# Optimization experiments

Measured on AMD Instinct MI355X. Metric: run time of the kernel, lower is better.

Reference implementation:

```python
import jax, jax.numpy as jnp
import numpy as np

TREE_DEPTH = 10
TOTAL = 2 ** (TREE_DEPTH + 1) - 1  # 2047 nodes per tree
G = 64                              # graphs per batch
N = G * TOTAL                       # 131008 nodes
E = 2 * N                           # 262016 directed edges
H = 256                             # h_dim
HALF = H // 2
L = 4                               # num_layers
LABELS = 32
OUT = 32
BN_EPS = 1e-5
LN_EPS = 1e-5


def setup_inputs() -> dict:
    key = jax.random.key(0)
    ks = jax.random.split(key, 16)
    x = jnp.stack([jax.random.randint(ks[0], (N,), 0, TOTAL),
                   jax.random.randint(ks[1], (N,), 0, LABELS)], axis=1)
    edge_src = jax.random.randint(ks[2], (E,), 0, N)
    edge_dst = jax.random.randint(ks[3], (E,), 0, N)
    edge_weight = jax.random.uniform(ks[4], (E,), dtype=jnp.float32)
    batch = jnp.arange(N, dtype=jnp.int64) // TOTAL          # node -> graph id
    root_index = jnp.arange(G, dtype=jnp.int64) * TOTAL      # one root per graph
    s = 0.02
    emb_node = jax.random.normal(ks[5], (TOTAL, HALF), dtype=jnp.float32) * s
    emb_label = jax.random.normal(ks[6], (LABELS, HALF), dtype=jnp.float32) * s
    w = 1.0 / np.sqrt(H)
    W1 = jax.random.normal(ks[7], (L, H, H), dtype=jnp.float32) * w
    b1 = jnp.zeros((L, H), dtype=jnp.float32)
    g1 = jnp.ones((L, H), dtype=jnp.float32)
    be1 = jnp.zeros((L, H), dtype=jnp.float32)
    W2 = jax.random.normal(ks[8], (L, H, H), dtype=jnp.float32) * w
    b2 = jnp.zeros((L, H), dtype=jnp.float32)
    g2 = jnp.ones((L, H), dtype=jnp.float32)
    be2 = jnp.zeros((L, H), dtype=jnp.float32)
    ln_g = jnp.ones((L, H), dtype=jnp.float32)
    ln_b = jnp.zeros((L, H), dtype=jnp.float32)
    Wout = jax.random.normal(ks[9], (OUT, H), dtype=jnp.float32) * w
    return {"x": x, "edge_src": edge_src, "edge_dst": edge_dst,
            "edge_weight": edge_weight, "batch": batch, "root_index": root_index,
            "emb_node": emb_node, "emb_label": emb_label,
            "W1": W1, "b1": b1, "g1": g1, "be1": be1,
            "W2": W2, "b2": b2, "g2": g2, "be2": be2,
            "ln_g": ln_g, "ln_b": ln_b, "Wout": Wout}


def _batchnorm(h, g, b):
    # BatchNorm1d, training-mode batch statistics over the node dim
    m = h.mean(axis=0)
    v = h.var(axis=0)
    return g * (h - m) * jax.lax.rsqrt(v + BN_EPS) + b


def _layernorm(h, g, b):
    m = h.mean(axis=-1, keepdims=True)
    v = h.var(axis=-1, keepdims=True)
    return g * (h - m) * jax.lax.rsqrt(v + LN_EPS) + b


def reference(x, edge_src, edge_dst, edge_weight, batch, root_index,
              emb_node, emb_label, W1, b1, g1, be1, W2, b2, g2, be2,
              ln_g, ln_b, Wout):
    # BiEmbedding_cat: concat of two h/2 embeddings
    h = jnp.concatenate([emb_node[x[:, 0]], emb_label[x[:, 1]]], axis=-1)  # [N,H]
    target_roots = root_index[batch]  # all-nodes->root targets for last layer
    for i in range(L):
        if i == L - 1:  # last_layer_fully_adjacent: every node sends to its root
            agg = jnp.zeros_like(h).at[target_roots].add(h)
        else:
            agg = jnp.zeros_like(h).at[edge_dst].add(h[edge_src] * edge_weight[:, None])
        m = h + agg  # GIN with eps=0: (1+eps)*x + sum_j w_ij x_j
        m = jax.nn.relu(_batchnorm(m @ W1[i].T + b1[i], g1[i], be1[i]))
        m = jax.nn.relu(_batchnorm(m @ W2[i].T + b2[i], g2[i], be2[i]))
        # use_activation: relu (idempotent after the MLP's trailing relu)
        h = h + m  # use_residual
        h = _layernorm(h, ln_g[i], ln_b[i])
    roots_x = h[root_index]  # [G,H] root readout
    return roots_x @ Wout.T  # [G,OUT], bias-free out layer
```

## Files before the change

kernel.cpp:

```cpp
#include <hip/hip_runtime.h>
#include <stdint.h>

#define NN 131008
#define NPAD 131072
#define EE 262016
#define HD 256
#define GG 64
#define TT 2047

typedef __attribute__((ext_vector_type(8))) short bfrag;
typedef __attribute__((ext_vector_type(4))) float f32x4;

__device__ __forceinline__ float bflo(unsigned u){ union{unsigned i; float f;} v; v.i = u<<16; return v.f; }
__device__ __forceinline__ float bfhi(unsigned u){ union{unsigned i; float f;} v; v.i = u & 0xffff0000u; return v.f; }
__device__ __forceinline__ unsigned short f2bf(float f){
  union{unsigned i; float fl;} v; v.fl = f; unsigned i = v.i;
  return (unsigned short)((i + 0x7fffu + ((i>>16)&1u)) >> 16);
}
__device__ __forceinline__ unsigned pack2(float a, float b){
  return (unsigned)f2bf(a) | ((unsigned)f2bf(b)<<16);
}
__device__ __forceinline__ void gload16(const void* g, void* s){
  __builtin_amdgcn_global_load_lds((__attribute__((address_space(1))) void*)g,
                                   (__attribute__((address_space(3))) void*)s, 16, 0, 0);
}

__device__ __forceinline__ short bnrelu1(short t, float a, float c){
  union{unsigned i; float f;} v; v.i = ((unsigned)(unsigned short)t) << 16;
  return (short)f2bf(fmaxf(a*v.f + c, 0.f));
}
__device__ __forceinline__ bfrag bn8(bfrag t, float4 a0, float4 a1, float4 c0, float4 c1){
  bfrag r;
  r[0]=bnrelu1(t[0],a0.x,c0.x); r[1]=bnrelu1(t[1],a0.y,c0.y);
  r[2]=bnrelu1(t[2],a0.z,c0.z); r[3]=bnrelu1(t[3],a0.w,c0.w);
  r[4]=bnrelu1(t[4],a1.x,c1.x); r[5]=bnrelu1(t[5],a1.y,c1.y);
  r[6]=bnrelu1(t[6],a1.z,c1.z); r[7]=bnrelu1(t[7],a1.w,c1.w);
  return r;
}

__device__ __forceinline__ void atomic_add_bf16x2(unsigned short* p, float a, float b){
#if __has_builtin(__builtin_amdgcn_global_atomic_fadd_v2bf16)
  typedef __attribute__((ext_vector_type(2))) short s16x2;
  s16x2 v; v.x = (short)f2bf(a); v.y = (short)f2bf(b);
  __builtin_amdgcn_global_atomic_fadd_v2bf16((__attribute__((address_space(1))) s16x2*)p, v);
#else
  unsigned* up = (unsigned*)p;
  unsigned old = *up, assumed;
  do {
    assumed = old;
    unsigned nv = pack2(bflo(assumed) + a, bfhi(assumed) + b);
    old = atomicCAS(up, assumed, nv);
  } while (old != assumed);
#endif
}

__global__ void k_prep(const float* __restrict__ W1, const float* __restrict__ W2,
                       unsigned short* __restrict__ wbf,
                       const int* __restrict__ x, const float* __restrict__ en,
                       const float* __restrict__ el, unsigned short* __restrict__ hbf,
                       const int* __restrict__ ed, int* __restrict__ deg){
  int b = blockIdx.x;
  if (b < 2048){
    int idx = b*256 + threadIdx.x;
    float v = (idx < 262144) ? W1[idx] : W2[idx - 262144];
    wbf[idx] = f2bf(v);
  } else if (b < 18432){
    size_t i8 = ((size_t)(b - 2048)*256 + threadIdx.x) << 3;
    int row = (int)(i8 >> 8); int k = (int)(i8 & 255);
    uint4 o;
    if (row < NN){
      const float* src = (k < 128) ? en + (size_t)x[2*row]*128 + k
                                   : el + (size_t)x[2*row+1]*128 + (k-128);
      float4 v0 = *(const float4*)src;
      float4 v1 = *(const float4*)(src + 4);
      o.x = pack2(v0.x, v0.y); o.y = pack2(v0.z, v0.w);
      o.z = pack2(v1.x, v1.y); o.w = pack2(v1.z, v1.w);
    } else { o.x = o.y = o.z = o.w = 0u; }
    *(uint4*)(hbf + i8) = o;
  } else {
    int e = (b - 18432)*256 + threadIdx.x;
    if (e < EE) atomicAdd(&deg[ed[e]], 1);
  }
}

__global__ void k_scan_block(const int* __restrict__ deg, int* __restrict__ start,
                             int* __restrict__ bsum){
  __shared__ int sh[256];
  int t = threadIdx.x;
  int i = blockIdx.x*256 + t;
  int v = deg[i];
  int val = v; sh[t] = val; __syncthreads();
  for (int off = 1; off < 256; off <<= 1){
    int add = (t >= off) ? sh[t-off] : 0;
    __syncthreads();
    val += add; sh[t] = val;
    __syncthreads();
  }
  start[i] = val - v;
  if (t == 255) bsum[blockIdx.x] = val;
}
__global__ void k_scan_top(int* __restrict__ bsum){
  __shared__ int sh[512];
  int t = threadIdx.x;
  int v = bsum[t];
  int val = v; sh[t] = val; __syncthreads();
  for (int off = 1; off < 512; off <<= 1){
    int add = (t >= off) ? sh[t-off] : 0;
    __syncthreads();
    val += add; sh[t] = val;
    __syncthreads();
  }
  bsum[t] = val - v;
}
__global__ void k_fill(const int* __restrict__ es, const int* __restrict__ ed,
                       const float* __restrict__ ew, const int* __restrict__ start,
                       const int* __restrict__ bsum,
                       int* __restrict__ cursor0, uint2* __restrict__ pairs){
  int e = blockIdx.x*256 + threadIdx.x;
  if (e < EE){
    int d = ed[e];
    int pos = start[d] + bsum[d >> 8] + atomicAdd(&cursor0[d], 1);
    uint2 p; p.x = (unsigned)es[e];
    union{float f; unsigned u;} w; w.f = ew[e];
    p.y = w.u;
    pairs[pos] = p;
  }
}

__global__ void k_gather(const int* __restrict__ deg, const int* __restrict__ start,
                         const int* __restrict__ bsum,
                         const uint2* __restrict__ pairs,
                         const unsigned short* __restrict__ hbf,
                         unsigned short* __restrict__ mbf){
  int half = threadIdx.x >> 5, lane32 = threadIdx.x & 31;
  int row = blockIdx.x*8 + half;
  size_t base = (size_t)row*HD + (lane32 << 3);
  uint4 o;
  if (row < NN){
    uint4 hv = *(const uint4*)(hbf + base);
    float a0 = bflo(hv.x), a1 = bfhi(hv.x), a2 = bflo(hv.y), a3 = bfhi(hv.y);
    float a4 = bflo(hv.z), a5 = bfhi(hv.z), a6 = bflo(hv.w), a7 = bfhi(hv.w);
    int d = deg[row], s = start[row] + bsum[row >> 8];
    for (int j = 0; j < d; ++j){
      uint2 pr = pairs[s + j];
      union{unsigned u; float f;} wg; wg.u = pr.y;
      uint4 sv = *(const uint4*)(hbf + (size_t)pr.x*HD + (lane32 << 3));
      a0 += bflo(sv.x)*wg.f; a1 += bfhi(sv.x)*wg.f;
      a2 += bflo(sv.y)*wg.f; a3 += bfhi(sv.y)*wg.f;
      a4 += bflo(sv.z)*wg.f; a5 += bfhi(sv.z)*wg.f;
      a6 += bflo(sv.w)*wg.f; a7 += bfhi(sv.w)*wg.f;
    }
    o.x = pack2(a0, a1); o.y = pack2(a2, a3);
    o.z = pack2(a4, a5); o.w = pack2(a6, a7);
  } else { o.x = o.y = o.z = o.w = 0u; }
  *(uint4*)(mbf + base) = o;
}

__global__ void k_rootsum(const unsigned short* __restrict__ hbf, unsigned short* __restrict__ m){
  int g = blockIdx.x >> 4, ch = blockIdx.x & 15;
  int col = threadIdx.x * 2;
  int nr = (ch == 15) ? 127 : 128;
  const unsigned short* p = hbf + ((size_t)g*TT + ch*128)*HD + col;
  float a = 0.f, b = 0.f;
  for (int r = 0; r < nr; ++r){
    unsigned u = *(const unsigned*)(p + (size_t)r*HD);
    a += bflo(u); b += bfhi(u);
  }
  atomic_add_bf16x2(m + (size_t)g*TT*HD + col, a, b);
}

template<bool TRANS>
__device__ __forceinline__ void gemm_body(const unsigned short* __restrict__ A,
                                          const unsigned short* __restrict__ B,
                                          unsigned short* __restrict__ C,
                                          float* __restrict__ gsum, float* __restrict__ gsq,
                                          const float* __restrict__ sum1,
                                          const float* __restrict__ sq1,
                                          const float* __restrict__ g1v,
                                          const float* __restrict__ be1v){
  __shared__ unsigned short Bs[65536];
  __shared__ unsigned short Ar[3*4096];
  __shared__ float acf[256];
  __shared__ float ccf[256];
  const int tid = threadIdx.x, lane = tid & 63, w = tid >> 6;
  const int wr = w >> 2, wc = w & 3;
  const int b = blockIdx.x;
  const int q = lane >> 4, r15 = lane & 15, r7 = lane & 7;
  const int NTS = 32;

  if (TRANS && tid < 256){
    const float inv_n = 1.f/(float)NN;
    float mean = sum1[tid] * inv_n;
    float var  = fmaxf(sq1[tid] * inv_n - mean*mean, 0.f);
    float aj   = g1v[tid] * rsqrtf(var + 1e-5f);
    acf[tid] = aj;
    ccf[tid] = be1v[tid] - aj*mean;
  }

#pragma unroll
  for (int kt = 0; kt < 4; ++kt)
#pragma unroll
    for (int it = 0; it < 4; ++it){
      int ci = it*512 + tid;
      int row = ci >> 3, cp = ci & 7;
      int cl = cp ^ (row & 7);
      gload16(B + (size_t)row*HD + kt*64 + cl*8, &Bs[kt*16384 + ci*8]);
    }
  {
    const int row = tid >> 2, cp = tid & 3;
    gload16(A + ((size_t)(b*4)*128 + row)*HD + 0*32 + cp*8, &Ar[0*4096 + tid*8]);
    gload16(A + ((size_t)(b*4)*128 + row)*HD + 1*32 + cp*8, &Ar[1*4096 + tid*8]);
  }

  f32x4 acc[4][4];
  f32x4 zz = {0.f, 0.f, 0.f, 0.f};
#pragma unroll
  for (int a = 0; a < 4; ++a)
#pragma unroll
    for (int c = 0; c < 4; ++c) acc[a][c] = zz;
  float cs[4] = {0.f,0.f,0.f,0.f}, cq[4] = {0.f,0.f,0.f,0.f};

  for (int s = 0; s < NTS; ++s){
    const int slot = s % 3;
    if (s == NTS-1) asm volatile("s_waitcnt vmcnt(0)" ::: "memory");
    else            asm volatile("s_waitcnt vmcnt(1)" ::: "memory");
    asm volatile("s_waitcnt lgkmcnt(0)" ::: "memory");
    __builtin_amdgcn_s_barrier();
    __builtin_amdgcn_sched_barrier(0);

    if (s + 2 < NTS){
      const int c = s + 2;
      const int tile2 = b*4 + (c >> 3), ks2 = c & 7;
      const int row = tid >> 2, cp = tid & 3;
      gload16(A + ((size_t)tile2*128 + row)*HD + ks2*32 + cp*8,
              &Ar[(c % 3)*4096 + tid*8]);
    }

    if (TRANS){
      const int ks = s & 7;
      const int kb = ks*32 + (tid & 3)*8;
      bfrag v = *(const bfrag*)&Ar[slot*4096 + tid*8];
      float4 a0 = *(const float4*)&acf[kb];
      float4 a1 = *(const float4*)&acf[kb + 4];
      float4 c0 = *(const float4*)&ccf[kb];
      float4 c1 = *(const float4*)&ccf[kb + 4];
      *(bfrag*)&Ar[slot*4096 + tid*8] = bn8(v, a0, a1, c0, c1);
      asm volatile("s_waitcnt lgkmcnt(0)" ::: "memory");
      __builtin_amdgcn_s_barrier();
      __builtin_amdgcn_sched_barrier(0);
    }

    const int kt64 = (s >> 1) & 3, hf = s & 1;
    bfrag af[4], bf[4];
#pragma unroll
    for (int rt = 0; rt < 4; ++rt){
      int ra = wr*64 + rt*16 + r15;
      af[rt] = *(const bfrag*)&Ar[slot*4096 + ra*32 + (q << 3)];
    }
#pragma unroll
    for (int ct = 0; ct < 4; ++ct){
      int rb = wc*64 + ct*16 + r15;
      bf[ct] = *(const bfrag*)&Bs[kt64*16384 + rb*64 + (((q + 4*hf) ^ r7) << 3)];
    }
#pragma unroll
    for (int rt = 0; rt < 4; ++rt)
#pragma unroll
      for (int ct = 0; ct < 4; ++ct)
        acc[rt][ct] = __builtin_amdgcn_mfma_f32_16x16x32_bf16(af[rt], bf[ct], acc[rt][ct], 0, 0, 0);

    if ((s & 7) == 7){
      const int tile = b*4 + (s >> 3);
      const int lr0 = wr*64 + q*4;
      const int lc0 = wc*64 + r15;
#pragma unroll
      for (int rt = 0; rt < 4; ++rt)
#pragma unroll
        for (int ct = 0; ct < 4; ++ct){
#pragma unroll
          for (int i = 0; i < 4; ++i){
            size_t grow = (size_t)tile*128 + lr0 + rt*16 + i;
            float v = acc[rt][ct][i];
            C[grow*HD + lc0 + ct*16] = f2bf(v);
            if (grow < NN){ cs[ct] += v; cq[ct] += v*v; }
          }
          acc[rt][ct] = zz;
        }
    }
  }

  __syncthreads();
  float* st = (float*)Ar;
  st[tid < 512 ? tid : 0] = 0.f;
  __syncthreads();
  const int lc0 = wc*64 + r15;
#pragma unroll
  for (int ct = 0; ct < 4; ++ct){
    float s2 = cs[ct], q2 = cq[ct];
    s2 += __shfl_xor(s2, 16); s2 += __shfl_xor(s2, 32);
    q2 += __shfl_xor(q2, 16); q2 += __shfl_xor(q2, 32);
    if (q == 0){
      atomicAdd(&st[lc0 + ct*16], s2);
      atomicAdd(&st[256 + lc0 + ct*16], q2);
    }
  }
  __syncthreads();
  if (tid < 256){
    atomicAdd(&gsum[tid], st[tid]);
    atomicAdd(&gsq[tid], st[256 + tid]);
  }
}

__global__ __launch_bounds__(512) void k_gemm(const unsigned short* __restrict__ A,
                                              const unsigned short* __restrict__ B,
                                              unsigned short* __restrict__ C,
                                              float* __restrict__ gsum, float* __restrict__ gsq){
  gemm_body<false>(A, B, C, gsum, gsq, nullptr, nullptr, nullptr, nullptr);
}
__global__ __launch_bounds__(512) void k_gemm2(const unsigned short* __restrict__ T,
                                               const float* __restrict__ sum1,
                                               const float* __restrict__ sq1,
                                               const float* __restrict__ g1v,
                                               const float* __restrict__ be1v,
                                               const unsigned short* __restrict__ B,
                                               unsigned short* __restrict__ C,
                                               float* __restrict__ gsum, float* __restrict__ gsq){
  gemm_body<true>(T, B, C, gsum, gsq, sum1, sq1, g1v, be1v);
}

__device__ __forceinline__ void coef4(float4 s4, float4 q4, float4 g4, float4 b4,
                                      float4& a, float4& c){
  const float inv_n = 1.f/(float)NN;
  float m0 = s4.x*inv_n, m1 = s4.y*inv_n, m2 = s4.z*inv_n, m3 = s4.w*inv_n;
  float i0 = rsqrtf(fmaxf(q4.x*inv_n - m0*m0, 0.f) + 1e-5f);
  float i1 = rsqrtf(fmaxf(q4.y*inv_n - m1*m1, 0.f) + 1e-5f);
  float i2 = rsqrtf(fmaxf(q4.z*inv_n - m2*m2, 0.f) + 1e-5f);
  float i3 = rsqrtf(fmaxf(q4.w*inv_n - m3*m3, 0.f) + 1e-5f);
  a.x = g4.x*i0; a.y = g4.y*i1; a.z = g4.z*i2; a.w = g4.w*i3;
  c.x = b4.x - a.x*m0; c.y = b4.y - a.y*m1; c.z = b4.z - a.z*m2; c.w = b4.w - a.w*m3;
}

__global__ void k_fuse(const unsigned short* t2,
                       const float* __restrict__ sum, const float* __restrict__ sq,
                       const float* __restrict__ g, const float* __restrict__ be,
                       const float* __restrict__ lg, const float* __restrict__ lb,
                       unsigned short* __restrict__ hbf, unsigned short* mbf,
                       int writem){
  int half = threadIdx.x >> 5, lane32 = threadIdx.x & 31;
  size_t row = (size_t)blockIdx.x*8 + half;
  int col = lane32 << 3;
  size_t base = row*HD + col;
  uint4 o;
  if (row < NN){
    float4 av0, cv0, av1, cv1;
    coef4(*(const float4*)(sum + col),     *(const float4*)(sq + col),
          *(const float4*)(g + col),       *(const float4*)(be + col),     av0, cv0);
    coef4(*(const float4*)(sum + col + 4), *(const float4*)(sq + col + 4),
          *(const float4*)(g + col + 4),   *(const float4*)(be + col + 4), av1, cv1);
    uint4 tv = *(const uint4*)(t2 + base);
    uint4 hv = *(const uint4*)(hbf + base);
    float r0 = bflo(hv.x) + fmaxf(av0.x*bflo(tv.x) + cv0.x, 0.f);
    float r1 = bfhi(hv.x) + fmaxf(av0.y*bfhi(tv.x) + cv0.y, 0.f);
    float r2 = bflo(hv.y) + fmaxf(av0.z*bflo(tv.y) + cv0.z, 0.f);
    float r3 = bfhi(hv.y) + fmaxf(av0.w*bfhi(tv.y) + cv0.w, 0.f);
    float r4 = bflo(hv.z) + fmaxf(av1.x*bflo(tv.z) + cv1.x, 0.f);
    float r5 = bfhi(hv.z) + fmaxf(av1.y*bfhi(tv.z) + cv1.y, 0.f);
    float r6 = bflo(hv.w) + fmaxf(av1.z*bflo(tv.w) + cv1.z, 0.f);
    float r7 = bfhi(hv.w) + fmaxf(av1.w*bfhi(tv.w) + cv1.w, 0.f);
    float s  = r0+r1+r2+r3+r4+r5+r6+r7;
    float qq = r0*r0+r1*r1+r2*r2+r3*r3+r4*r4+r5*r5+r6*r6+r7*r7;
#pragma unroll
    for (int d = 1; d < 32; d <<= 1){ s += __shfl_xor(s, d); qq += __shfl_xor(qq, d); }
    float mean = s * (1.f/256.f);
    float var  = fmaxf(qq * (1.f/256.f) - mean*mean, 0.f);
    float inv  = rsqrtf(var + 1e-5f);
    float4 gv0 = *(const float4*)(lg + col), gv1 = *(const float4*)(lg + col + 4);
    float4 bv0 = *(const float4*)(lb + col), bv1 = *(const float4*)(lb + col + 4);
    o.x = pack2(gv0.x*(r0 - mean)*inv + bv0.x, gv0.y*(r1 - mean)*inv + bv0.y);
    o.y = pack2(gv0.z*(r2 - mean)*inv + bv0.z, gv0.w*(r3 - mean)*inv + bv0.w);
    o.z = pack2(gv1.x*(r4 - mean)*inv + bv1.x, gv1.y*(r5 - mean)*inv + bv1.y);
    o.w = pack2(gv1.z*(r6 - mean)*inv + bv1.z, gv1.w*(r7 - mean)*inv + bv1.w);
  } else {
    o.x = o.y = o.z = o.w = 0u;
  }
  *(uint4*)(hbf + base) = o;
  if (writem) *(uint4*)(mbf + base) = o;
}

__global__ void k_readout(const unsigned short* __restrict__ hbf, const float* __restrict__ Wo,
                          float* __restrict__ out){
  int g = blockIdx.x;
  int w = threadIdx.x >> 6, lane = threadIdx.x & 63;
  uint2 hv = *(const uint2*)(hbf + (size_t)g*TT*HD + (lane<<2));
  float h0 = bflo(hv.x), h1 = bfhi(hv.x), h2 = bflo(hv.y), h3 = bfhi(hv.y);
#pragma unroll
  for (int oo = 0; oo < 8; ++oo){
    int o = w*8 + oo;
    float4 wv = *(const float4*)(Wo + (size_t)o*HD + (lane<<2));
    float p = h0*wv.x + h1*wv.y + h2*wv.z + h3*wv.w;
#pragma unroll
    for (int d = 1; d < 64; d <<= 1) p += __shfl_xor(p, d);
    if (lane == 0) out[g*32 + o] = p;
  }
}

extern "C" void kernel_launch(void* const* d_in, const int* in_sizes, int n_in,
                              void* d_out, int out_size, void* d_ws, size_t ws_size,
                              hipStream_t stream){
  const int*   x   = (const int*)d_in[0];
  const int*   es  = (const int*)d_in[1];
  const int*   ed  = (const int*)d_in[2];
  const float* ew  = (const float*)d_in[3];
  const float* en  = (const float*)d_in[6];
  const float* el  = (const float*)d_in[7];
  const float* W1  = (const float*)d_in[8];
  const float* g1  = (const float*)d_in[10];
  const float* be1 = (const float*)d_in[11];
  const float* W2  = (const float*)d_in[12];
  const float* g2  = (const float*)d_in[14];
  const float* be2 = (const float*)d_in[15];
  const float* lg  = (const float*)d_in[16];
  const float* lb  = (const float*)d_in[17];
  const float* Wo  = (const float*)d_in[18];

  char* ws = (char*)d_ws;
  unsigned short* hbf = (unsigned short*)ws;
  unsigned short* mbf = (unsigned short*)(ws + 67108864);
  unsigned short* t   = (unsigned short*)(ws + 134217728);
  unsigned short* wbf = (unsigned short*)(ws + 201326592);
  float* stats   = (float*)(ws + 202375168);
  int*   deg     = (int*)  (ws + 202391552);
  int*   cursor0 = (int*)  (ws + 202915840);
  int*   start   = (int*)  (ws + 203440128);
  int*   bsum    = (int*)  (ws + 203964416);
  uint2* pairs   = (uint2*)(ws + 203968512);

  hipMemsetAsync(stats, 0, 16384 + 524288 + 524288, stream);
  k_prep<<<19456, 256, 0, stream>>>(W1, W2, wbf, x, en, el, hbf, ed, deg);

  k_scan_block<<<512, 256, 0, stream>>>(deg, start, bsum);
  k_scan_top  <<<1,   512, 0, stream>>>(bsum);
  k_fill      <<<1024,256, 0, stream>>>(es, ed, ew, start, bsum, cursor0, pairs);

  for (int i = 0; i < 4; ++i){
    float* s1 = stats + (2*i)*512;
    float* s2 = stats + (2*i+1)*512;
    if (i < 3) k_gather <<<16384, 256, 0, stream>>>(deg, start, bsum, pairs, hbf, mbf);
    else       k_rootsum<<<1024,  128, 0, stream>>>(hbf, mbf);

    k_gemm <<<256, 512, 0, stream>>>(mbf, wbf + i*65536, t, s1, s1 + 256);
    k_gemm2<<<256, 512, 0, stream>>>(t, s1, s1 + 256, g1 + i*256, be1 + i*256,
                                     wbf + 262144 + i*65536, mbf, s2, s2 + 256);
    k_fuse <<<16384, 256, 0, stream>>>(mbf, s2, s2 + 256, g2 + i*256, be2 + i*256,
                                       lg + i*256, lb + i*256, hbf, mbf, (i == 2) ? 1 : 0);
  }

  k_readout<<<64, 256, 0, stream>>>(hbf, Wo, (float*)d_out);
  (void)in_sizes; (void)n_in; (void)out_size; (void)ws_size;
}
```

Baseline: 807.9 us.

## Load GEMM A fragments directly to registers, drop LDS staging and per-step barriers

The GEMM no longer stages A tiles through LDS with a three-slot ring and per-step barriers. Each wave now loads its own A fragments straight from global memory into registers, prefetching three k-steps ahead in a four-slot register ring, and applies the BN transform in registers. The wave layout changes from 2x4 to 4x2, so each wave covers 32 rows by 128 columns, and s_setprio is raised around the MFMA block. This removes barrier and LDS round-trip overhead from the main loop, but it costs more registers and gives up A reuse across waves, so each A element is loaded twice from global memory.

After: 754.3 us. 1.07x faster.

```diff
diff --git a/kernel.cpp b/kernel.cpp
--- a/kernel.cpp
+++ b/kernel.cpp
@@ -179,14 +179,13 @@
                                           const float* __restrict__ g1v,
                                           const float* __restrict__ be1v){
   __shared__ unsigned short Bs[65536];
-  __shared__ unsigned short Ar[3*4096];
+  __shared__ float st[512];
   __shared__ float acf[256];
   __shared__ float ccf[256];
   const int tid = threadIdx.x, lane = tid & 63, w = tid >> 6;
-  const int wr = w >> 2, wc = w & 3;
+  const int wr = w >> 1, wc = w & 1;
   const int b = blockIdx.x;
   const int q = lane >> 4, r15 = lane & 15, r7 = lane & 7;
-  const int NTS = 32;
 
   if (TRANS && tid < 256){
     const float inv_n = 1.f/(float)NN;
@@ -196,6 +195,7 @@
     acf[tid] = aj;
     ccf[tid] = be1v[tid] - aj*mean;
   }
+  st[tid < 512 ? tid : 0] = 0.f;
 
 #pragma unroll
   for (int kt = 0; kt < 4; ++kt)
@@ -206,76 +206,66 @@
       int cl = cp ^ (row & 7);
       gload16(B + (size_t)row*HD + kt*64 + cl*8, &Bs[kt*16384 + ci*8]);
     }
-  {
-    const int row = tid >> 2, cp = tid & 3;
-    gload16(A + ((size_t)(b*4)*128 + row)*HD + 0*32 + cp*8, &Ar[0*4096 + tid*8]);
-    gload16(A + ((size_t)(b*4)*128 + row)*HD + 1*32 + cp*8, &Ar[1*4096 + tid*8]);
-  }
-
-  f32x4 acc[4][4];
+
+  bfrag rA[4][2];
+  auto aload = [&](int s, int slot){
+    const int t2 = b*4 + (s >> 3), ks = s & 7;
+    const unsigned short* p = A + ((size_t)(t2*128 + wr*32 + r15))*HD + ks*32 + (q << 3);
+    rA[slot][0] = *(const bfrag*)p;
+    rA[slot][1] = *(const bfrag*)(p + 16*HD);
+  };
+  aload(0, 0); aload(1, 1); aload(2, 2);
+
+  asm volatile("s_waitcnt vmcnt(0) lgkmcnt(0)" ::: "memory");
+  __builtin_amdgcn_s_barrier();
+
+  f32x4 acc[2][8];
   f32x4 zz = {0.f, 0.f, 0.f, 0.f};
 #pragma unroll
-  for (int a = 0; a < 4; ++a)
-#pragma unroll
-    for (int c = 0; c < 4; ++c) acc[a][c] = zz;
-  float cs[4] = {0.f,0.f,0.f,0.f}, cq[4] = {0.f,0.f,0.f,0.f};
-
-  for (int s = 0; s < NTS; ++s){
-    const int slot = s % 3;
-    if (s == NTS-1) asm volatile("s_waitcnt vmcnt(0)" ::: "memory");
-    else            asm volatile("s_waitcnt vmcnt(1)" ::: "memory");
-    asm volatile("s_waitcnt lgkmcnt(0)" ::: "memory");
-    __builtin_amdgcn_s_barrier();
-    __builtin_amdgcn_sched_barrier(0);
-
-    if (s + 2 < NTS){
-      const int c = s + 2;
-      const int tile2 = b*4 + (c >> 3), ks2 = c & 7;
-      const int row = tid >> 2, cp = tid & 3;
-      gload16(A + ((size_t)tile2*128 + row)*HD + ks2*32 + cp*8,
-              &Ar[(c % 3)*4096 + tid*8]);
-    }
-
+  for (int a = 0; a < 2; ++a)
+#pragma unroll
+    for (int c = 0; c < 8; ++c) acc[a][c] = zz;
+  float cs[8] = {0,0,0,0,0,0,0,0}, cq[8] = {0,0,0,0,0,0,0,0};
+
+#pragma unroll 4
+  for (int s = 0; s < 32; ++s){
+    if (s < 29) aload(s + 3, (s + 3) & 3);
+
+    bfrag a0 = rA[s & 3][0], a1 = rA[s & 3][1];
+    const int ks = s & 7;
     if (TRANS){
-      const int ks = s & 7;
-      const int kb = ks*32 + (tid & 3)*8;
-      bfrag v = *(const bfrag*)&Ar[slot*4096 + tid*8];
-      float4 a0 = *(const float4*)&acf[kb];
-      float4 a1 = *(const float4*)&acf[kb + 4];
-      float4 c0 = *(const float4*)&ccf[kb];
-      float4 c1 = *(const float4*)&ccf[kb + 4];
-      *(bfrag*)&Ar[slot*4096 + tid*8] = bn8(v, a0, a1, c0, c1);
-      asm volatile("s_waitcnt lgkmcnt(0)" ::: "memory");
-      __builtin_amdgcn_s_barrier();
-      __builtin_amdgcn_sched_barrier(0);
-    }
-
-    const int kt64 = (s >> 1) & 3, hf = s & 1;
-    bfrag af[4], bf[4];
-#pragma unroll
-    for (int rt = 0; rt < 4; ++rt){
-      int ra = wr*64 + rt*16 + r15;
-      af[rt] = *(const bfrag*)&Ar[slot*4096 + ra*32 + (q << 3)];
-    }
-#pragma unroll
-    for (int ct = 0; ct < 4; ++ct){
-      int rb = wc*64 + ct*16 + r15;
+      const int kb = ks*32 + (q << 3);
+      float4 ca0 = *(const float4*)&acf[kb];
+      float4 ca1 = *(const float4*)&acf[kb + 4];
+      float4 cc0 = *(const float4*)&ccf[kb];
+      float4 cc1 = *(const float4*)&ccf[kb + 4];
+      a0 = bn8(a0, ca0, ca1, cc0, cc1);
+      a1 = bn8(a1, ca0, ca1, cc0, cc1);
+    }
+
+    const int kt64 = ks >> 1, hf = ks & 1;
+    bfrag bf[8];
+#pragma unroll
+    for (int ct = 0; ct < 8; ++ct){
+      int rb = wc*128 + ct*16 + r15;
       bf[ct] = *(const bfrag*)&Bs[kt64*16384 + rb*64 + (((q + 4*hf) ^ r7) << 3)];
     }
-#pragma unroll
-    for (int rt = 0; rt < 4; ++rt)
-#pragma unroll
-      for (int ct = 0; ct < 4; ++ct)
-        acc[rt][ct] = __builtin_amdgcn_mfma_f32_16x16x32_bf16(af[rt], bf[ct], acc[rt][ct], 0, 0, 0);
+    __builtin_amdgcn_s_setprio(1);
+#pragma unroll
+    for (int ct = 0; ct < 8; ++ct){
+      acc[0][ct] = __builtin_amdgcn_mfma_f32_16x16x32_bf16(a0, bf[ct], acc[0][ct], 0, 0, 0);
+      acc[1][ct] = __builtin_amdgcn_mfma_f32_16x16x32_bf16(a1, bf[ct], acc[1][ct], 0, 0, 0);
+    }
+    __builtin_amdgcn_s_setprio(0);
 
     if ((s & 7) == 7){
       const int tile = b*4 + (s >> 3);
-      const int lr0 = wr*64 + q*4;
-      const int lc0 = wc*64 + r15;
-#pragma unroll
-      for (int rt = 0; rt < 4; ++rt)
-#pragma unroll
-        for (int ct = 0; ct < 4; ++ct){
+      const int lr0 = wr*32 + q*4;
+      const int lc0 = wc*128 + r15;
+#pragma unroll
+      for (int rt = 0; rt < 2; ++rt)
+#pragma unroll
+        for (int ct = 0; ct < 8; ++ct){
 #pragma unroll
           for (int i = 0; i < 4; ++i){
             size_t grow = (size_t)tile*128 + lr0 + rt*16 + i;
@@ -288,13 +278,9 @@
     }
   }
 
-  __syncthreads();
-  float* st = (float*)Ar;
-  st[tid < 512 ? tid : 0] = 0.f;
-  __syncthreads();
-  const int lc0 = wc*64 + r15;
-#pragma unroll
-  for (int ct = 0; ct < 4; ++ct){
+  const int lc0 = wc*128 + r15;
+#pragma unroll
+  for (int ct = 0; ct < 8; ++ct){
     float s2 = cs[ct], q2 = cq[ct];
     s2 += __shfl_xor(s2, 16); s2 += __shfl_xor(s2, 32);
     q2 += __shfl_xor(q2, 16); q2 += __shfl_xor(q2, 32);
```
